# Performance work log

Measured on AMD Instinct MI355X. Metric: run time of the kernel, lower is better.

## Reference

```python
import jax, jax.numpy as jnp
import numpy as np

T = 2.0  # __init__ arg t (temperature exponent); logits scaled by exp(t)


def setup_inputs() -> dict:
    key = jax.random.key(0)
    k1, k2 = jax.random.split(key)
    N = 4096
    logits_per_image = jax.random.normal(k1, (N, N), dtype=jnp.float32)
    labels = jax.random.randint(k2, (N,), 0, 512, dtype=jnp.int64)
    return {"logits_per_image": logits_per_image, "labels": labels}


def reference(logits_per_image, labels):
    # p[i,j] = softmax over row i of (logits * exp(t))
    N = logits_per_image.shape[0]
    p = jax.nn.softmax(logits_per_image * jnp.exp(jnp.float32(T)), axis=1)
    # mask[i,j] = 1 iff i==j or labels[i] != labels[j]; loss uses
    #   log p[i,i] on the diagonal, mask * log(1 - p[i,j]) off-diagonal.
    diag_term = jnp.sum(jnp.log(jnp.diagonal(p)))
    neq = (labels[:, None] != labels[None, :]).astype(p.dtype)  # zero on diagonal
    off_term = jnp.sum(neq * jnp.log1p(-p))
    return (diag_term + off_term) / N
```

## Files before the change

kernel.cpp:

```cpp
#include <hip/hip_runtime.h>

#define N_DIM 4096
#define SCALE 7.3890560989306495f

__global__ __launch_bounds__(256, 8) void minfonce_kernel(
    const float* __restrict__ logits,
    const int*   __restrict__ labels,
    float*       __restrict__ out)
{
    const int tid  = threadIdx.x;
    const int lane = tid & 63;
    const int wv   = tid >> 6;
    const int half = wv & 1;
    const int row  = (blockIdx.x << 1) + (wv >> 1);
    const int g0   = half << 3;

    __shared__ int4  slab[N_DIM / 4];
    __shared__ float sS[4], sX[4], sM[4], sA[4];

    const int4* lp = reinterpret_cast<const int4*>(labels);
#pragma unroll
    for (int j = 0; j < 4; ++j) slab[tid + 256 * j] = lp[tid + 256 * j];
    __syncthreads();

    const float4* rp = reinterpret_cast<const float4*>(logits + (size_t)row * N_DIM);
    const int     li = reinterpret_cast<const int*>(slab)[row];

    float m8[8];
    float s_all = 0.f, s_mask = 0.f;
#pragma unroll
    for (int g = 0; g < 8; ++g) {
        const float4 t  = rp[lane + 64 * (g0 + g)];
        const int4   lb = slab[lane + 64 * (g0 + g)];
        const float ex = __expf(SCALE * t.x);
        const float ey = __expf(SCALE * t.y);
        const float ez = __expf(SCALE * t.z);
        const float ew = __expf(SCALE * t.w);
        s_all  += (ex + ey) + (ez + ew);
        s_mask += ((lb.x != li ? ex : 0.f) + (lb.y != li ? ey : 0.f))
                + ((lb.z != li ? ez : 0.f) + (lb.w != li ? ew : 0.f));
        m8[g] = fmaxf(fmaxf(ex, ey), fmaxf(ez, ew));
    }
    float emax = m8[0];
#pragma unroll
    for (int g = 1; g < 8; ++g) emax = fmaxf(emax, m8[g]);

#pragma unroll
    for (int off = 1; off < 64; off <<= 1) {
        s_all  += __shfl_xor(s_all, off);
        s_mask += __shfl_xor(s_mask, off);
        emax    = fmaxf(emax, __shfl_xor(emax, off));
    }
    if (lane == 0) { sS[wv] = s_all; sX[wv] = s_mask; sM[wv] = emax; }
    __syncthreads();

    const int  w0    = wv & ~1;
    const float S     = sS[w0] + sS[w0 | 1];
    const float Smask = sX[w0] + sX[w0 | 1];
    const float Emax  = fmaxf(sM[w0], sM[w0 | 1]);
    const float invS  = 1.0f / S;
    const float tau   = 1e-3f * S;
    const float qmax  = fmaxf(S - Emax, S * 1e-12f) * invS;

    float acc = 0.f;
#pragma unroll
    for (int g = 0; g < 8; ++g) {
        if (m8[g] > tau) {
            const float4 t  = rp[lane + 64 * (g0 + g)];
            const int4   lb = slab[lane + 64 * (g0 + g)];
            { const float ev = __expf(SCALE * t.x);
              if (ev > tau && lb.x != li) {
                  const float p = ev * invS;
                  const float q = (ev == Emax) ? qmax : (1.0f - p);
                  acc += __logf(q) + p; } }
            { const float ev = __expf(SCALE * t.y);
              if (ev > tau && lb.y != li) {
                  const float p = ev * invS;
                  const float q = (ev == Emax) ? qmax : (1.0f - p);
                  acc += __logf(q) + p; } }
            { const float ev = __expf(SCALE * t.z);
              if (ev > tau && lb.z != li) {
                  const float p = ev * invS;
                  const float q = (ev == Emax) ? qmax : (1.0f - p);
                  acc += __logf(q) + p; } }
            { const float ev = __expf(SCALE * t.w);
              if (ev > tau && lb.w != li) {
                  const float p = ev * invS;
                  const float q = (ev == Emax) ? qmax : (1.0f - p);
                  acc += __logf(q) + p; } }
        }
    }

    if (half == 0 && lane == 0)
        acc += (SCALE * logits[(size_t)row * N_DIM + row] - __logf(S))
             - Smask * invS;

#pragma unroll
    for (int off = 1; off < 64; off <<= 1)
        acc += __shfl_xor(acc, off);

    if (lane == 0) sA[wv] = acc;
    __syncthreads();
    if (tid == 0) {
        const float total = (sA[0] + sA[1]) + (sA[2] + sA[3]);
        atomicAdd(out, total * (1.0f / N_DIM));
    }
}

extern "C" void kernel_launch(void* const* d_in, const int* in_sizes, int n_in,
                              void* d_out, int out_size, void* d_ws, size_t ws_size,
                              hipStream_t stream) {
    const float* logits = (const float*)d_in[0];
    const int*   labels = (const int*)d_in[1];
    float*       out    = (float*)d_out;

    hipMemsetAsync(out, 0, sizeof(float), stream);
    minfonce_kernel<<<N_DIM / 2, 256, 0, stream>>>(logits, labels, out);
}
```

Measured before the change: 117.0 us.

## Hoist all row and label loads into registers, drop shared label staging

Removes the shared-memory staging of the full labels array and its block barrier. Each wave now issues all eight float4 logit loads and eight int4 label loads up front, with a scheduling barrier so they stay in flight together, and keeps them in registers for both passes instead of re-reading the row in the fix-up pass. This raises register use, so launch bounds drop from 8 to 4 blocks per CU, trading occupancy for memory-level parallelism and less redundant traffic. Labels now come from global/L2 for every block instead of LDS.

```diff
diff --git a/kernel.cpp b/kernel.cpp
--- a/kernel.cpp
+++ b/kernel.cpp
@@ -3,7 +3,7 @@
 #define N_DIM 4096
 #define SCALE 7.3890560989306495f
 
-__global__ __launch_bounds__(256, 8) void minfonce_kernel(
+__global__ __launch_bounds__(256, 4) void minfonce_kernel(
     const float* __restrict__ logits,
     const int*   __restrict__ labels,
     float*       __restrict__ out)
@@ -13,34 +13,40 @@
     const int wv   = tid >> 6;
     const int half = wv & 1;
     const int row  = (blockIdx.x << 1) + (wv >> 1);
-    const int g0   = half << 3;
 
-    __shared__ int4  slab[N_DIM / 4];
     __shared__ float sS[4], sX[4], sM[4], sA[4];
 
-    const int4* lp = reinterpret_cast<const int4*>(labels);
-#pragma unroll
-    for (int j = 0; j < 4; ++j) slab[tid + 256 * j] = lp[tid + 256 * j];
-    __syncthreads();
+    const float4* rp = reinterpret_cast<const float4*>(logits + (size_t)row * N_DIM);
+    const int4*   lp = reinterpret_cast<const int4*>(labels);
+    const int     li = labels[row];
+    const int     i0 = lane + (half << 9);
 
-    const float4* rp = reinterpret_cast<const float4*>(logits + (size_t)row * N_DIM);
-    const int     li = reinterpret_cast<const int*>(slab)[row];
+    const float4 u0 = rp[i0 +   0]; const int4 b0 = lp[i0 +   0];
+    const float4 u1 = rp[i0 +  64]; const int4 b1 = lp[i0 +  64];
+    const float4 u2 = rp[i0 + 128]; const int4 b2 = lp[i0 + 128];
+    const float4 u3 = rp[i0 + 192]; const int4 b3 = lp[i0 + 192];
+    const float4 u4 = rp[i0 + 256]; const int4 b4 = lp[i0 + 256];
+    const float4 u5 = rp[i0 + 320]; const int4 b5 = lp[i0 + 320];
+    const float4 u6 = rp[i0 + 384]; const int4 b6 = lp[i0 + 384];
+    const float4 u7 = rp[i0 + 448]; const int4 b7 = lp[i0 + 448];
+    __builtin_amdgcn_sched_barrier(0);
 
     float m8[8];
     float s_all = 0.f, s_mask = 0.f;
-#pragma unroll
-    for (int g = 0; g < 8; ++g) {
-        const float4 t  = rp[lane + 64 * (g0 + g)];
-        const int4   lb = slab[lane + 64 * (g0 + g)];
-        const float ex = __expf(SCALE * t.x);
-        const float ey = __expf(SCALE * t.y);
-        const float ez = __expf(SCALE * t.z);
-        const float ew = __expf(SCALE * t.w);
-        s_all  += (ex + ey) + (ez + ew);
-        s_mask += ((lb.x != li ? ex : 0.f) + (lb.y != li ? ey : 0.f))
-                + ((lb.z != li ? ez : 0.f) + (lb.w != li ? ew : 0.f));
-        m8[g] = fmaxf(fmaxf(ex, ey), fmaxf(ez, ew));
-    }
+#define ACCG(G, T, B) do {                                             \
+        const float ex = __expf(SCALE * T.x);                          \
+        const float ey = __expf(SCALE * T.y);                          \
+        const float ez = __expf(SCALE * T.z);                          \
+        const float ew = __expf(SCALE * T.w);                          \
+        s_all  += (ex + ey) + (ez + ew);                               \
+        s_mask += ((B.x != li ? ex : 0.f) + (B.y != li ? ey : 0.f))    \
+                + ((B.z != li ? ez : 0.f) + (B.w != li ? ew : 0.f));   \
+        m8[G] = fmaxf(fmaxf(ex, ey), fmaxf(ez, ew));                   \
+    } while (0)
+    ACCG(0, u0, b0); ACCG(1, u1, b1); ACCG(2, u2, b2); ACCG(3, u3, b3);
+    ACCG(4, u4, b4); ACCG(5, u5, b5); ACCG(6, u6, b6); ACCG(7, u7, b7);
+#undef ACCG
+
     float emax = m8[0];
 #pragma unroll
     for (int g = 1; g < 8; ++g) emax = fmaxf(emax, m8[g]);
@@ -54,7 +60,7 @@
     if (lane == 0) { sS[wv] = s_all; sX[wv] = s_mask; sM[wv] = emax; }
     __syncthreads();
 
-    const int  w0    = wv & ~1;
+    const int   w0    = wv & ~1;
     const float S     = sS[w0] + sS[w0 | 1];
     const float Smask = sX[w0] + sX[w0 | 1];
     const float Emax  = fmaxf(sM[w0], sM[w0 | 1]);
@@ -63,33 +69,18 @@
     const float qmax  = fmaxf(S - Emax, S * 1e-12f) * invS;
 
     float acc = 0.f;
-#pragma unroll
-    for (int g = 0; g < 8; ++g) {
-        if (m8[g] > tau) {
-            const float4 t  = rp[lane + 64 * (g0 + g)];
-            const int4   lb = slab[lane + 64 * (g0 + g)];
-            { const float ev = __expf(SCALE * t.x);
-              if (ev > tau && lb.x != li) {
-                  const float p = ev * invS;
-                  const float q = (ev == Emax) ? qmax : (1.0f - p);
-                  acc += __logf(q) + p; } }
-            { const float ev = __expf(SCALE * t.y);
-              if (ev > tau && lb.y != li) {
-                  const float p = ev * invS;
-                  const float q = (ev == Emax) ? qmax : (1.0f - p);
-                  acc += __logf(q) + p; } }
-            { const float ev = __expf(SCALE * t.z);
-              if (ev > tau && lb.z != li) {
-                  const float p = ev * invS;
-                  const float q = (ev == Emax) ? qmax : (1.0f - p);
-                  acc += __logf(q) + p; } }
-            { const float ev = __expf(SCALE * t.w);
-              if (ev > tau && lb.w != li) {
-                  const float p = ev * invS;
-                  const float q = (ev == Emax) ? qmax : (1.0f - p);
-                  acc += __logf(q) + p; } }
-        }
-    }
+#define FIX1(X, L) {                                                   \
+        const float ev = __expf(SCALE * (X));                          \
+        if (ev > tau && (L) != li) {                                   \
+            const float p = ev * invS;                                 \
+            const float q = (ev == Emax) ? qmax : (1.0f - p);          \
+            acc += __logf(q) + p; } }
+#define FIXG(G, T, B) if (m8[G] > tau) {                               \
+        FIX1(T.x, B.x) FIX1(T.y, B.y) FIX1(T.z, B.z) FIX1(T.w, B.w) }
+    FIXG(0, u0, b0); FIXG(1, u1, b1); FIXG(2, u2, b2); FIXG(3, u3, b3);
+    FIXG(4, u4, b4); FIXG(5, u5, b5); FIXG(6, u6, b6); FIXG(7, u7, b7);
+#undef FIXG
+#undef FIX1
 
     if (half == 0 && lane == 0)
         acc += (SCALE * logits[(size_t)row * N_DIM + row] - __logf(S))
```

New measurement: 115.2 us. About the same (-1.6%).
